# Performance work log

Measured on AMD Instinct MI355X. Metric: run time of the kernel, lower is better.

## Reference

```python
import jax, jax.numpy as jnp
import numpy as np

B, N, IN_DIM, HID, EMB, E = 64, 2048, 128, 256, 64, 4194304
TOTAL = B * N


def _init(key, shape, fan_in):
    return jax.random.normal(key, shape, jnp.float32) / np.sqrt(fan_in).astype(np.float32)


def setup_inputs() -> dict:
    key = jax.random.key(0)
    ks = jax.random.split(key, 9)
    x = jax.random.normal(ks[0], (TOTAL, IN_DIM), jnp.float32)
    src = jax.random.randint(ks[1], (E,), 0, TOTAL)
    dst = jax.random.randint(ks[2], (E,), 0, TOTAL)
    return {
        "x": x,
        "src": src,
        "dst": dst,
        "num_nodes": TOTAL,
        "nodes_per_graph": N,
        "w_lin": _init(ks[3], (IN_DIM, HID), IN_DIM),
        "b_lin": jnp.zeros((HID,), jnp.float32),
        "w_c0": _init(ks[4], (HID, HID), HID),
        "b_c0": jnp.zeros((HID,), jnp.float32),
        "w_c1": _init(ks[5], (HID, HID), HID),
        "b_c1": jnp.zeros((HID,), jnp.float32),
        "w_emb": _init(ks[6], (HID, EMB), HID),
        "b_emb": jnp.zeros((EMB,), jnp.float32),
    }


def reference(x, src, dst, num_nodes, nodes_per_graph,
              w_lin, b_lin, w_c0, b_c0, w_c1, b_c1, w_emb, b_emb):
    # DGL GraphConv norm='both': deg clamped to min 1, symmetric normalization
    ones = jnp.ones(src.shape, x.dtype)
    out_deg = jax.ops.segment_sum(ones, src, num_segments=num_nodes)
    in_deg = jax.ops.segment_sum(ones, dst, num_segments=num_nodes)
    out_norm = jnp.maximum(out_deg, 1.0) ** -0.5  # [num_nodes]
    in_norm = jnp.maximum(in_deg, 1.0) ** -0.5

    def graph_conv(h, W, b):
        hs = h * out_norm[:, None]                                   # pre-norm by out-degree
        agg = jax.ops.segment_sum(hs[src], dst, num_segments=num_nodes)  # SpMM: sum messages
        return (agg * in_norm[:, None]) @ W + b                      # post-norm, then weight

    h = jax.nn.relu(x @ w_lin + b_lin)          # [total, HID]
    h = jax.nn.relu(graph_conv(h, w_c0, b_c0))  # residual=False for agg_style='node'
    h = jax.nn.relu(graph_conv(h, w_c1, b_c1))
    # agent node 0 of each graph in the batch: indices 0, N, 2N, ...
    agent = h[jnp.arange(0, num_nodes, nodes_per_graph)]  # [B, HID]
    return agent @ w_emb + b_emb                          # [B, EMB]
```

## Files before the change

kernel.cpp:

```cpp
#include <hip/hip_runtime.h>
#include <hip/hip_bf16.h>

#define TOTAL_N   131072
#define NEDGE     4194304
#define NPG       2048
#define IN_DIM_K  128
#define HID_K     256
#define EMB_K     64
#define NAGENT    64

#define F1CAP     4096
#define APACK     128
#define BCAP      96

#define G1        256
#define EPB1      (NEDGE / G1)
#define HWORDS    (TOTAL_N / 8)

#define SELB      256
#define EPB       (NEDGE / SELB)


#define ZERO_SPAN 34048

typedef float f32x4 __attribute__((ext_vector_type(4)));
typedef short bf16x8 __attribute__((ext_vector_type(8)));

__device__ inline unsigned short f2bf(float f) {
    unsigned int u = __float_as_uint(f);
    return (unsigned short)((u + 0x7FFFu + ((u >> 16) & 1u)) >> 16);
}

__global__ __launch_bounds__(1024) void k_outdeg_e0(
    const int* __restrict__ src, const int* __restrict__ dst,
    unsigned int* __restrict__ partial,
    unsigned int* __restrict__ bitmap,
    int* __restrict__ e0pack, int* __restrict__ e0cnt)
{
    __shared__ unsigned int hist[HWORDS];
    int t = threadIdx.x;
    #pragma unroll
    for (int i = 0; i < HWORDS / 1024; i++) hist[t + i * 1024] = 0u;
    __syncthreads();

    int ebase = blockIdx.x * EPB1;
    const int4* s4 = (const int4*)(src + ebase);
    const int4* d4 = (const int4*)(dst + ebase);
    #pragma unroll
    for (int i = 0; i < EPB1 / 4096; i++) {
        int4 sv = s4[i * 1024 + t];
        int4 dv = d4[i * 1024 + t];
        int ss[4] = {sv.x, sv.y, sv.z, sv.w};
        int dd[4] = {dv.x, dv.y, dv.z, dv.w};
        #pragma unroll
        for (int j = 0; j < 4; j++) {
            int s = ss[j], d = dd[j];
            atomicAdd(&hist[s >> 3], 1u << ((s & 7) * 4));
            if ((d & (NPG - 1)) == 0) {
                atomicOr(&bitmap[s >> 5], 1u << (s & 31));
                int a = d >> 11;
                int slot = atomicAdd(&e0cnt[a], 1);
                if (slot < APACK) e0pack[a * APACK + slot] = s;
            }
        }
    }
    __syncthreads();
    unsigned int* pout = partial + blockIdx.x * HWORDS;
    #pragma unroll
    for (int i = 0; i < HWORDS / 1024; i++) pout[t + i * 1024] = hist[t + i * 1024];
}

__global__ __launch_bounds__(1024) void k_auxred(
    const unsigned int* __restrict__ bitmap, int* __restrict__ loc,
    int* __restrict__ counters,
    const unsigned int* __restrict__ partial, unsigned int* __restrict__ out_deg,
    const float* __restrict__ wlin, unsigned short* __restrict__ wswz)
{
    int b = blockIdx.x;
    int t = threadIdx.x;
    if (b < 128) {
        __shared__ int cnt, gbase;
        if (t == 0) cnt = 0;
        __syncthreads();
        int v = b * 1024 + t;
        int f = (bitmap[v >> 5] >> (v & 31)) & 1u;
        int p = -1;
        if (f) p = atomicAdd(&cnt, 1);
        __syncthreads();
        if (t == 0) gbase = cnt ? atomicAdd(&counters[1], cnt) : 0;
        __syncthreads();
        int l = -1;
        if (p >= 0) { int id = gbase + p; if (id < F1CAP) l = id; }
        loc[v] = l;
    } else if (b < 256) {
        __shared__ unsigned int redE[8][128], redO[8][128];
        int wl = t & 127, gs = t >> 7;
        int w = (b - 128) * 128 + wl;
        unsigned int accE = 0, accO = 0;
        #pragma unroll 8
        for (int i = 0; i < 32; i++) {
            unsigned int v = partial[(gs * 32 + i) * HWORDS + w];
            accE += v & 0x0F0F0F0Fu;
            accO += (v >> 4) & 0x0F0F0F0Fu;
        }
        redE[gs][wl] = accE;
        redO[gs][wl] = accO;
        __syncthreads();
        if (gs == 0) {
            unsigned int sE = 0, sO = 0;
            #pragma unroll
            for (int j = 0; j < 8; j++) { sE += redE[j][wl]; sO += redO[j][wl]; }
            uint4 lo = make_uint4(sE & 255u, sO & 255u, (sE >> 8) & 255u, (sO >> 8) & 255u);
            uint4 hi = make_uint4((sE >> 16) & 255u, (sO >> 16) & 255u, (sE >> 24) & 255u, (sO >> 24) & 255u);
            ((uint4*)(out_deg + 8 * w))[0] = lo;
            ((uint4*)(out_deg + 8 * w))[1] = hi;
        }
    } else {
        int g = (b - 256) * 1024 + t;
        int lane = g & 63, ct = (g >> 6) & 15, kt = g >> 10;
        int colbase = ct * 16 + (lane & 15);
        int kbase = kt * 32 + (lane >> 4) * 8;
        unsigned short o[8];
        #pragma unroll
        for (int i = 0; i < 8; i++) o[i] = f2bf(wlin[(kbase + i) * HID_K + colbase]);
        *(ushort4*)(wswz + g * 8)     = make_ushort4(o[0], o[1], o[2], o[3]);
        *(ushort4*)(wswz + g * 8 + 4) = make_ushort4(o[4], o[5], o[6], o[7]);
    }
}

__global__ __launch_bounds__(1024) void k_e1_select(
    const int* __restrict__ src, const int* __restrict__ dst,
    const int* __restrict__ loc, const unsigned int* __restrict__ bitmap,
    int* __restrict__ inF1, int* __restrict__ es_bucket)
{
    __shared__ unsigned int bm[TOTAL_N / 32];
    int t = threadIdx.x;
    ((uint4*)bm)[t] = ((const uint4*)bitmap)[t];
    __syncthreads();

    int ebase = blockIdx.x * EPB;
    const int4* d4p = (const int4*)(dst + ebase);
    #pragma unroll
    for (int i = 0; i < EPB / 4096; i++) {
        int4 d4 = d4p[i * 1024 + t];
        int eidx = ebase + (i * 1024 + t) * 4;
        int dd[4] = {d4.x, d4.y, d4.z, d4.w};
        #pragma unroll
        for (int j = 0; j < 4; j++) {
            int d = dd[j];
            if ((bm[d >> 5] >> (d & 31)) & 1u) {
                int l = loc[d];
                if (l >= 0) {
                    int slot = atomicAdd(&inF1[l], 1);
                    if (slot < BCAP) es_bucket[l * BCAP + slot] = src[eidx + j];
                }
            }
        }
    }
}

__global__ __launch_bounds__(256) void k_h0agg(
    const float* __restrict__ x, const unsigned short* __restrict__ wswz,
    const float* __restrict__ blin, const int* __restrict__ es_bucket,
    const unsigned int* __restrict__ out_deg, const int* __restrict__ inF1,
    const int* __restrict__ counters, float* __restrict__ agg1)
{
    __shared__ unsigned short A[4][32][136];
    __shared__ float escs[4][32];
    __shared__ int rsrc[4][32];

    int nF1 = min(counters[1], F1CAP);
    int t = threadIdx.x;
    int w = t >> 6, lane = t & 63;
    int l = blockIdx.x * 4 + w;
    if (l >= nF1) return;
    int cnt = min(inF1[l], BCAP);
    int ntile = (cnt + 31) >> 5;
    int cbase = lane & 15, rgrp = (lane >> 4) * 4;

    float bj[16];
    #pragma unroll
    for (int n = 0; n < 16; n++) bj[n] = blin[n * 16 + cbase];

    float colacc[16];
    #pragma unroll
    for (int n = 0; n < 16; n++) colacc[n] = 0.f;

    for (int ti = 0; ti < ntile; ti++) {
        if (lane < 32) {
            int r = ti * 32 + lane;
            int s = (r < cnt) ? es_bucket[l * BCAP + r] : -1;
            rsrc[w][lane] = s;
            escs[w][lane] = (s >= 0) ? rsqrtf((float)max((int)out_deg[s], 1)) : 0.f;
        }
        #pragma unroll
        for (int i = 0; i < 16; i++) {
            int idx = lane + i * 64;
            int r2 = idx >> 5, q = idx & 31;
            int s2 = rsrc[w][r2];
            float4 v = make_float4(0.f, 0.f, 0.f, 0.f);
            if (s2 >= 0) v = ((const float4*)(x + (long long)s2 * IN_DIM_K))[q];
            ushort4 h;
            h.x = f2bf(v.x); h.y = f2bf(v.y); h.z = f2bf(v.z); h.w = f2bf(v.w);
            *(ushort4*)&A[w][r2][q * 4] = h;
        }
        bf16x8 a0[4], a1[4];
        const unsigned short* Ab = &A[w][0][0];
        #pragma unroll
        for (int kt = 0; kt < 4; kt++) {
            a0[kt] = *(const bf16x8*)(Ab + ((lane & 15) * 136 + kt * 32 + (lane >> 4) * 8));
            a1[kt] = *(const bf16x8*)(Ab + (((lane & 15) + 16) * 136 + kt * 32 + (lane >> 4) * 8));
        }
        #pragma unroll
        for (int n = 0; n < 16; n++) {
            f32x4 acc0 = (f32x4){0.f, 0.f, 0.f, 0.f};
            f32x4 acc1 = (f32x4){0.f, 0.f, 0.f, 0.f};
            #pragma unroll
            for (int kt = 0; kt < 4; kt++) {
                bf16x8 bf = *(const bf16x8*)(wswz + ((kt * 16 + n) * 64 + lane) * 8);
                acc0 = __builtin_amdgcn_mfma_f32_16x16x32_bf16(a0[kt], bf, acc0, 0, 0, 0);
                acc1 = __builtin_amdgcn_mfma_f32_16x16x32_bf16(a1[kt], bf, acc1, 0, 0, 0);
            }
            float part = 0.f;
            #pragma unroll
            for (int j = 0; j < 4; j++) {
                part += fmaxf(acc0[j] + bj[n], 0.f) * escs[w][rgrp + j];
                part += fmaxf(acc1[j] + bj[n], 0.f) * escs[w][16 + rgrp + j];
            }
            part += __shfl_xor(part, 16);
            part += __shfl_xor(part, 32);
            colacc[n] += part;
        }
    }

    if (lane < 16) {
        #pragma unroll
        for (int n = 0; n < 16; n++)
            agg1[(long long)l * HID_K + n * 16 + lane] = colacc[n];
    }
}

__global__ __launch_bounds__(256) void k_h1(
    const float* __restrict__ agg1, const float* __restrict__ wc0,
    const float* __restrict__ bc0,
    const int* __restrict__ inF1,
    const int* __restrict__ counters, float* __restrict__ h1)
{
    __shared__ float as[16][HID_K];
    __shared__ float ns[16];

    int nF1 = min(counters[1], F1CAP);
    int rt = blockIdx.x >> 2;
    int cq = blockIdx.x & 3;
    int base = rt * 16;
    if (base >= nF1) return;
    int t = threadIdx.x;

    if (t < 16) {
        int l = base + t;
        ns[t] = (l < nF1) ? rsqrtf((float)max(inF1[l], 1)) : 0.f;
    }
    __syncthreads();

    #pragma unroll
    for (int i = 0; i < 4; i++) {
        int idx = t + i * 256;
        int e = idx >> 6;
        int q = idx & 63;
        int l = base + e;
        float4 v = make_float4(0.f, 0.f, 0.f, 0.f);
        if (l < nF1) v = ((const float4*)(agg1 + (long long)l * HID_K))[q];
        float sc = ns[e];
        v.x *= sc; v.y *= sc; v.z *= sc; v.w *= sc;
        ((float4*)as[e])[q] = v;
    }
    __syncthreads();

    int j = cq * 64 + (t & 63);
    int rg = (t >> 6) * 4;
    float acc[4] = {0.f, 0.f, 0.f, 0.f};

    for (int k = 0; k < HID_K; k += 4) {
        float w0 = wc0[(k + 0) * HID_K + j];
        float w1 = wc0[(k + 1) * HID_K + j];
        float w2 = wc0[(k + 2) * HID_K + j];
        float w3 = wc0[(k + 3) * HID_K + j];
        #pragma unroll
        for (int e = 0; e < 4; e++) {
            float4 av = *(const float4*)&as[rg + e][k];
            acc[e] = fmaf(av.x, w0, acc[e]);
            acc[e] = fmaf(av.y, w1, acc[e]);
            acc[e] = fmaf(av.z, w2, acc[e]);
            acc[e] = fmaf(av.w, w3, acc[e]);
        }
    }

    float bj = bc0[j];
    #pragma unroll
    for (int e = 0; e < 4; e++) {
        int l = base + rg + e;
        if (l < nF1) h1[(long long)l * HID_K + j] = fmaxf(acc[e] + bj, 0.f);
    }
}

__global__ __launch_bounds__(1024) void k_final(
    const int* __restrict__ e0pack, const int* __restrict__ e0cnt,
    const int* __restrict__ loc, const unsigned int* __restrict__ out_deg,
    const float* __restrict__ h1,
    const float* __restrict__ wc1, const float* __restrict__ bc1,
    const float* __restrict__ wemb, const float* __restrict__ bemb,
    float* __restrict__ out)
{
    __shared__ float part4[4][HID_K];
    __shared__ float a_s[HID_K];
    __shared__ float h2[HID_K];
    __shared__ float o_part[16][EMB_K];
    __shared__ int   ls[APACK];
    __shared__ float scs[APACK];
    int a = blockIdx.x;
    int t = threadIdx.x;

    int n0 = e0cnt[a];
    int ne = min(n0, APACK);
    if (t < ne) {
        int s = e0pack[a * APACK + t];
        int l = loc[s];
        ls[t] = l;
        scs[t] = (l >= 0) ? rsqrtf((float)max((int)out_deg[s], 1)) : 0.f;
    }
    __syncthreads();

    {
        int col = t & 255, sl = t >> 8;
        float acc = 0.f;
        for (int i = sl; i < ne; i += 4) {
            int l = ls[i];
            if (l >= 0) acc = fmaf(scs[i], h1[(long long)l * HID_K + col], acc);
        }
        part4[sl][col] = acc;
    }
    __syncthreads();
    if (t < HID_K) {
        float s = part4[0][t] + part4[1][t] + part4[2][t] + part4[3][t];
        a_s[t] = s * rsqrtf((float)max(n0, 1));
    }
    __syncthreads();

    {
        int col = t & 255, sl = t >> 8;
        float acc = 0.f;
        int k0 = sl * 64;
        for (int k = k0; k < k0 + 64; k++)
            acc = fmaf(a_s[k], wc1[k * HID_K + col], acc);
        part4[sl][col] = acc;
    }
    __syncthreads();
    if (t < HID_K) {
        float s = part4[0][t] + part4[1][t] + part4[2][t] + part4[3][t];
        h2[t] = fmaxf(s + bc1[t], 0.f);
    }
    __syncthreads();

    {
        int col = t & 63, sl = t >> 6;
        float acc = 0.f;
        int k0 = sl * 16;
        for (int k = k0; k < k0 + 16; k++)
            acc = fmaf(h2[k], wemb[k * EMB_K + col], acc);
        o_part[sl][col] = acc;
    }
    __syncthreads();
    if (t < EMB_K) {
        float o = bemb[t];
        #pragma unroll
        for (int s = 0; s < 16; s++) o += o_part[s][t];
        out[a * EMB_K + t] = o;
    }
}

extern "C" void kernel_launch(void* const* d_in, const int* in_sizes, int n_in,
                              void* d_out, int out_size, void* d_ws, size_t ws_size,
                              hipStream_t stream)
{
    const float* x    = (const float*)d_in[0];
    const int*   src  = (const int*)d_in[1];
    const int*   dst  = (const int*)d_in[2];
    const float* wlin = (const float*)d_in[5];
    const float* blin = (const float*)d_in[6];
    const float* wc0  = (const float*)d_in[7];
    const float* bc0  = (const float*)d_in[8];
    const float* wc1  = (const float*)d_in[9];
    const float* bc1  = (const float*)d_in[10];
    const float* wemb = (const float*)d_in[11];
    const float* bemb = (const float*)d_in[12];
    float* out = (float*)d_out;

    char* ws = (char*)d_ws;
    int*            counters  = (int*)(ws + 0);
    int*            inF1      = (int*)(ws + 1024);
    int*            e0cnt     = (int*)(ws + 17408);
    unsigned int*   bitmap    = (unsigned int*)(ws + 17664);
    int*            loc       = (int*)(ws + 65536);
    int*            e0pack    = (int*)(ws + 589824);
    int*            es_bucket = (int*)(ws + 622592);
    unsigned int*   out_deg   = (unsigned int*)(ws + 2195456);
    unsigned short* wswz      = (unsigned short*)(ws + 2719744);
    float*          h1        = (float*)(ws + 2785280);
    float*          agg1      = (float*)(ws + 6979584);
    unsigned int*   partial   = (unsigned int*)(ws + 11173888);

    hipMemsetAsync(ws, 0, ZERO_SPAN, stream);

    k_outdeg_e0<<<G1, 1024, 0, stream>>>(src, dst, partial, bitmap, e0pack, e0cnt);
    k_auxred<<<260, 1024, 0, stream>>>(bitmap, loc, counters,
                                       partial, out_deg, wlin, wswz);
    k_e1_select<<<SELB, 1024, 0, stream>>>(src, dst, loc, bitmap,
                                           inF1, es_bucket);
    k_h0agg<<<F1CAP / 4, 256, 0, stream>>>(x, wswz, blin, es_bucket, out_deg,
                                           inF1, counters, agg1);
    k_h1<<<(F1CAP / 16) * 4, 256, 0, stream>>>(agg1, wc0, bc0, inF1,
                                               counters, h1);
    k_final<<<NAGENT, 1024, 0, stream>>>(e0pack, e0cnt, loc, out_deg, h1,
                                         wc1, bc1, wemb, bemb, out);
}
```

Measured before the change: 108.6 us.

## Pre-convert x to bf16 in the degree kernel and gather MFMA operands directly

Extra blocks appended to the out-degree kernel convert the whole x matrix to bf16 in workspace. The first aggregation kernel then loads bf16 rows straight from global memory into MFMA A-operand registers, using shuffles to hand out row indices and norms. This drops the LDS staging buffer, the per-element conversion and half the bytes of the random row gather. In exchange it adds a full streaming read of x plus a half-size write, which it hopes to overlap with the atomic-bound histogram blocks.

```diff
diff --git a/kernel.cpp b/kernel.cpp
--- a/kernel.cpp
+++ b/kernel.cpp
@@ -33,17 +33,35 @@
 
 __global__ __launch_bounds__(1024) void k_outdeg_e0(
     const int* __restrict__ src, const int* __restrict__ dst,
+    const float* __restrict__ x,
     unsigned int* __restrict__ partial,
     unsigned int* __restrict__ bitmap,
-    int* __restrict__ e0pack, int* __restrict__ e0cnt)
+    int* __restrict__ e0pack, int* __restrict__ e0cnt,
+    unsigned short* __restrict__ xb)
 {
     __shared__ unsigned int hist[HWORDS];
     int t = threadIdx.x;
+    int b = blockIdx.x;
+
+    if (b >= G1) {
+        long long base = (long long)(b - G1) * 65536;
+        const float4* xi = (const float4*)(x + base);
+        ushort4* xo = (ushort4*)(xb + base);
+        #pragma unroll 4
+        for (int i = 0; i < 16; i++) {
+            float4 v = xi[i * 1024 + t];
+            ushort4 h;
+            h.x = f2bf(v.x); h.y = f2bf(v.y); h.z = f2bf(v.z); h.w = f2bf(v.w);
+            xo[i * 1024 + t] = h;
+        }
+        return;
+    }
+
     #pragma unroll
     for (int i = 0; i < HWORDS / 1024; i++) hist[t + i * 1024] = 0u;
     __syncthreads();
 
-    int ebase = blockIdx.x * EPB1;
+    int ebase = b * EPB1;
     const int4* s4 = (const int4*)(src + ebase);
     const int4* d4 = (const int4*)(dst + ebase);
     #pragma unroll
@@ -65,7 +83,7 @@
         }
     }
     __syncthreads();
-    unsigned int* pout = partial + blockIdx.x * HWORDS;
+    unsigned int* pout = partial + b * HWORDS;
     #pragma unroll
     for (int i = 0; i < HWORDS / 1024; i++) pout[t + i * 1024] = hist[t + i * 1024];
 }
@@ -160,15 +178,11 @@
 }
 
 __global__ __launch_bounds__(256) void k_h0agg(
-    const float* __restrict__ x, const unsigned short* __restrict__ wswz,
+    const unsigned short* __restrict__ xb, const unsigned short* __restrict__ wswz,
     const float* __restrict__ blin, const int* __restrict__ es_bucket,
     const unsigned int* __restrict__ out_deg, const int* __restrict__ inF1,
     const int* __restrict__ counters, float* __restrict__ agg1)
 {
-    __shared__ unsigned short A[4][32][136];
-    __shared__ float escs[4][32];
-    __shared__ int rsrc[4][32];
-
     int nF1 = min(counters[1], F1CAP);
     int t = threadIdx.x;
     int w = t >> 6, lane = t & 63;
@@ -177,40 +191,39 @@
     int cnt = min(inF1[l], BCAP);
     int ntile = (cnt + 31) >> 5;
     int cbase = lane & 15, rgrp = (lane >> 4) * 4;
-
-    float bj[16];
-    #pragma unroll
-    for (int n = 0; n < 16; n++) bj[n] = blin[n * 16 + cbase];
+    int ko = (lane >> 4) * 8;
 
     float colacc[16];
     #pragma unroll
     for (int n = 0; n < 16; n++) colacc[n] = 0.f;
 
+    const bf16x8 zf = {0, 0, 0, 0, 0, 0, 0, 0};
+
     for (int ti = 0; ti < ntile; ti++) {
-        if (lane < 32) {
-            int r = ti * 32 + lane;
-            int s = (r < cnt) ? es_bucket[l * BCAP + r] : -1;
-            rsrc[w][lane] = s;
-            escs[w][lane] = (s >= 0) ? rsqrtf((float)max((int)out_deg[s], 1)) : 0.f;
-        }
-        #pragma unroll
-        for (int i = 0; i < 16; i++) {
-            int idx = lane + i * 64;
-            int r2 = idx >> 5, q = idx & 31;
-            int s2 = rsrc[w][r2];
-            float4 v = make_float4(0.f, 0.f, 0.f, 0.f);
-            if (s2 >= 0) v = ((const float4*)(x + (long long)s2 * IN_DIM_K))[q];
-            ushort4 h;
-            h.x = f2bf(v.x); h.y = f2bf(v.y); h.z = f2bf(v.z); h.w = f2bf(v.w);
-            *(ushort4*)&A[w][r2][q * 4] = h;
-        }
+        int s = -1; float e = 0.f;
+        int r = ti * 32 + lane;
+        if (lane < 32 && r < cnt) {
+            s = es_bucket[l * BCAP + r];
+            e = rsqrtf((float)max((int)out_deg[s], 1));
+        }
+        int s0 = __shfl(s, cbase);
+        int s1 = __shfl(s, 16 + cbase);
+        float e0[4], e1[4];
+        #pragma unroll
+        for (int j = 0; j < 4; j++) {
+            e0[j] = __shfl(e, rgrp + j);
+            e1[j] = __shfl(e, 16 + rgrp + j);
+        }
+
         bf16x8 a0[4], a1[4];
-        const unsigned short* Ab = &A[w][0][0];
+        const unsigned short* x0 = xb + (long long)s0 * IN_DIM_K;
+        const unsigned short* x1 = xb + (long long)s1 * IN_DIM_K;
         #pragma unroll
         for (int kt = 0; kt < 4; kt++) {
-            a0[kt] = *(const bf16x8*)(Ab + ((lane & 15) * 136 + kt * 32 + (lane >> 4) * 8));
-            a1[kt] = *(const bf16x8*)(Ab + (((lane & 15) + 16) * 136 + kt * 32 + (lane >> 4) * 8));
-        }
+            a0[kt] = (s0 >= 0) ? *(const bf16x8*)(x0 + kt * 32 + ko) : zf;
+            a1[kt] = (s1 >= 0) ? *(const bf16x8*)(x1 + kt * 32 + ko) : zf;
+        }
+
         #pragma unroll
         for (int n = 0; n < 16; n++) {
             f32x4 acc0 = (f32x4){0.f, 0.f, 0.f, 0.f};
@@ -221,11 +234,12 @@
                 acc0 = __builtin_amdgcn_mfma_f32_16x16x32_bf16(a0[kt], bf, acc0, 0, 0, 0);
                 acc1 = __builtin_amdgcn_mfma_f32_16x16x32_bf16(a1[kt], bf, acc1, 0, 0, 0);
             }
+            float bj = blin[n * 16 + cbase];
             float part = 0.f;
             #pragma unroll
             for (int j = 0; j < 4; j++) {
-                part += fmaxf(acc0[j] + bj[n], 0.f) * escs[w][rgrp + j];
-                part += fmaxf(acc1[j] + bj[n], 0.f) * escs[w][16 + rgrp + j];
+                part += fmaxf(acc0[j] + bj, 0.f) * e0[j];
+                part += fmaxf(acc1[j] + bj, 0.f) * e1[j];
             }
             part += __shfl_xor(part, 16);
             part += __shfl_xor(part, 32);
@@ -408,15 +422,17 @@
     float*          h1        = (float*)(ws + 2785280);
     float*          agg1      = (float*)(ws + 6979584);
     unsigned int*   partial   = (unsigned int*)(ws + 11173888);
+    unsigned short* xb        = (unsigned short*)(ws + 27951104);
 
     hipMemsetAsync(ws, 0, ZERO_SPAN, stream);
 
-    k_outdeg_e0<<<G1, 1024, 0, stream>>>(src, dst, partial, bitmap, e0pack, e0cnt);
+    k_outdeg_e0<<<G1 + 256, 1024, 0, stream>>>(src, dst, x, partial, bitmap,
+                                               e0pack, e0cnt, xb);
     k_auxred<<<260, 1024, 0, stream>>>(bitmap, loc, counters,
                                        partial, out_deg, wlin, wswz);
     k_e1_select<<<SELB, 1024, 0, stream>>>(src, dst, loc, bitmap,
                                            inF1, es_bucket);
-    k_h0agg<<<F1CAP / 4, 256, 0, stream>>>(x, wswz, blin, es_bucket, out_deg,
+    k_h0agg<<<F1CAP / 4, 256, 0, stream>>>(xb, wswz, blin, es_bucket, out_deg,
                                            inF1, counters, agg1);
     k_h1<<<(F1CAP / 16) * 4, 256, 0, stream>>>(agg1, wc0, bc0, inF1,
                                                counters, h1);
```

Result: faster. 101.8 us, median of 2 (-6.2%).
